# Kernel optimization log

Hardware: AMD Instinct MI355X
Metric: run time of the kernel (lower is better)

## Reference

```python
import jax, jax.numpy as jnp
import numpy as np

N, E, D_IN, D_H, D_OUT = 50000, 800000, 128, 128, 64


def _glorot(key, shape):
    fan_in, fan_out = shape[1], shape[0]
    lim = (6.0 / (fan_in + fan_out)) ** 0.5
    return jax.random.uniform(key, shape, jnp.float32, -lim, lim)


def setup_inputs() -> dict:
    key = jax.random.key(0)
    ks = jax.random.split(key, 8)
    x = jax.random.normal(ks[0], (N, D_IN), jnp.float32)
    edge_index = jax.random.randint(ks[1], (2, E), 0, N, jnp.int64)
    # SAGEConv layer 1: lin_l (on aggregated neighbors, with bias) and lin_r (root, no bias)
    W1l = _glorot(ks[2], (D_H, D_IN))
    b1 = jnp.zeros((D_H,), jnp.float32)
    W1r = _glorot(ks[3], (D_H, D_IN))
    # SAGEConv layer 2
    W2l = _glorot(ks[4], (D_OUT, D_H))
    b2 = jnp.zeros((D_OUT,), jnp.float32)
    W2r = _glorot(ks[5], (D_OUT, D_H))
    return {"x": x, "edge_index": edge_index, "W1l": W1l, "b1": b1, "W1r": W1r,
            "W2l": W2l, "b2": b2, "W2r": W2r}


def _sage_conv(x, src, dst, inv_deg, Wl, b, Wr):
    # mean-aggregate neighbor features: gather x[src], scatter-sum into dst, divide by degree
    msg_sum = jax.ops.segment_sum(x[src], dst, num_segments=N)  # [N, d]
    agg = msg_sum * inv_deg[:, None]
    return agg @ Wl.T + b + x @ Wr.T


def reference(x, edge_index, W1l, b1, W1r, W2l, b2, W2r):
    src, dst = edge_index[0], edge_index[1]
    deg = jax.ops.segment_sum(jnp.ones((E,), jnp.float32), dst, num_segments=N)
    inv_deg = jnp.where(deg > 0, 1.0 / jnp.maximum(deg, 1.0), 0.0)
    h = _sage_conv(x, src, dst, inv_deg, W1l, b1, W1r)
    h = jax.nn.relu(h)  # dropout is identity in eval mode
    out = _sage_conv(h, src, dst, inv_deg, W2l, b2, W2r)
    return out
```

## Files before the change

### kernel.cpp

```cpp
#include <hip/hip_runtime.h>
#include <hip/hip_bf16.h>

typedef __hip_bfloat16 bf16;
typedef __attribute__((ext_vector_type(8))) short short8;
typedef __attribute__((ext_vector_type(4))) float f32x4;

#define N_NODES 50000
#define NE      800000
#define DIN     128
#define DH      128
#define DOUT    64
#define MTILES  (N_NODES / 16)
#define CAP     64

__device__ __forceinline__ int clamp_node(int s) {
    return min(max(s, 0), N_NODES - 1);
}
__device__ __forceinline__ float b2f(short s) {
    unsigned u = ((unsigned)(unsigned short)s) << 16;
    float f; __builtin_memcpy(&f, &u, 4); return f;
}
__device__ __forceinline__ short f2b(float f) {
    __hip_bfloat16 h = __float2bfloat16(f);
    short s; __builtin_memcpy(&s, &h, 2); return s;
}

__global__ void k_build(const int* __restrict__ src, const int* __restrict__ dst,
                        int* __restrict__ deg, int* __restrict__ csrPad,
                        const float* __restrict__ x, __hip_bfloat162* __restrict__ xb2,
                        const float* __restrict__ W1l, const float* __restrict__ W1r,
                        const float* __restrict__ W2l, const float* __restrict__ W2r,
                        bf16* __restrict__ W1b, bf16* __restrict__ W2b) {
    int b = blockIdx.x;
    if (b < 3125) {
        int e = b * 256 + threadIdx.x;
        int t = clamp_node(dst[e]);
        int pos = atomicAdd(&deg[t], 1);
        if (pos < CAP) csrPad[t * CAP + pos] = src[e];
    } else if (b < 3125 + 6250) {
        int i = (b - 3125) * 256 + threadIdx.x;
        float4 v = ((const float4*)x)[i];
        __hip_bfloat162 a, bb;
        a.x = __float2bfloat16(v.x); a.y = __float2bfloat16(v.y);
        bb.x = __float2bfloat16(v.z); bb.y = __float2bfloat16(v.w);
        xb2[2 * i]     = a;
        xb2[2 * i + 1] = bb;
    } else {
        int i = (b - 9375) * 256 + threadIdx.x;
        if (i < 128 * 256) {
            int n = i >> 8, k = i & 255;
            float v = (k < 128) ? W1l[n * 128 + k] : W1r[n * 128 + (k - 128)];
            W1b[i] = __float2bfloat16(v);
        } else {
            int j = i - 128 * 256;
            int n = j >> 7, k = j & 127;
            float v = (n < 64) ? W2l[n * 128 + k] : W2r[(n - 64) * 128 + k];
            W2b[j] = __float2bfloat16(v);
        }
    }
}

__global__ __launch_bounds__(256) void k_agg1(const int* __restrict__ deg, const int* __restrict__ csrPad,
                                              const short* __restrict__ xb,
                                              short* __restrict__ msg) {
    int node = blockIdx.x * 4 + (threadIdx.x >> 6);
    if (node >= N_NODES) return;
    int lane = threadIdx.x & 63;
    int g = lane >> 4, c = lane & 15;
    int d = min(max(deg[node], 0), CAP);
    int lo = node * CAP, hi = lo + d;
    float acc[8];
    #pragma unroll
    for (int j = 0; j < 8; ++j) acc[j] = 0.f;
    int i = lo;
    for (; i + 7 < hi; i += 8) {
        int n0 = clamp_node(csrPad[i + g]);
        int n1 = clamp_node(csrPad[i + 4 + g]);
        short8 v0 = *(const short8*)(xb + (size_t)n0 * DIN + c * 8);
        short8 v1 = *(const short8*)(xb + (size_t)n1 * DIN + c * 8);
        #pragma unroll
        for (int j = 0; j < 8; ++j) acc[j] += b2f(v0[j]) + b2f(v1[j]);
    }
    for (; i < hi; i += 4) {
        bool valid = (i + g) < hi;
        int n = clamp_node(csrPad[valid ? (i + g) : i]);
        short8 v = *(const short8*)(xb + (size_t)n * DIN + c * 8);
        if (valid) {
            #pragma unroll
            for (int j = 0; j < 8; ++j) acc[j] += b2f(v[j]);
        }
    }
    #pragma unroll
    for (int j = 0; j < 8; ++j) {
        acc[j] += __shfl_xor(acc[j], 16);
        acc[j] += __shfl_xor(acc[j], 32);
    }
    if (g == 0) {
        float inv = (d > 0) ? 1.0f / (float)d : 0.0f;
        short8 o;
        #pragma unroll
        for (int j = 0; j < 8; ++j) o[j] = f2b(acc[j] * inv);
        *(short8*)(msg + (size_t)node * DIN + c * 8) = o;
    }
}

__global__ __launch_bounds__(256) void k_mfma12(const short* __restrict__ msg,
                                                const short* __restrict__ xb,
                                                const short* __restrict__ W1b,
                                                const float* __restrict__ b1,
                                                const short* __restrict__ W2b,
                                                bf16* __restrict__ pb,
                                                float* __restrict__ qbuf) {
    __shared__ short hs[16][136];
    int wave = threadIdx.x >> 6, lane = threadIdx.x & 63;
    int q = lane >> 4, mr = lane & 15;
    int n0 = wave * 32;
    short8 Bf1[2][8];
    #pragma unroll
    for (int t = 0; t < 2; ++t) {
        const short* wrow = W1b + (size_t)(n0 + t * 16 + mr) * 256 + q * 8;
        #pragma unroll
        for (int ks = 0; ks < 8; ++ks) Bf1[t][ks] = *(const short8*)(wrow + ks * 32);
    }
    short8 Bf2[2][4];
    #pragma unroll
    for (int t = 0; t < 2; ++t) {
        const short* wrow = W2b + (size_t)(n0 + t * 16 + mr) * 128 + q * 8;
        #pragma unroll
        for (int ks = 0; ks < 4; ++ks) Bf2[t][ks] = *(const short8*)(wrow + ks * 32);
    }
    float bias0 = b1[n0 + mr], bias1 = b1[n0 + 16 + mr];
    for (int mt = blockIdx.x; mt < MTILES; mt += gridDim.x) {
        const short* a0 = msg + (size_t)(mt * 16 + mr) * DIN + q * 8;
        const short* a1 = xb  + (size_t)(mt * 16 + mr) * DIN + q * 8;
        short8 Af[8];
        #pragma unroll
        for (int ks = 0; ks < 4; ++ks) Af[ks]     = *(const short8*)(a0 + ks * 32);
        #pragma unroll
        for (int ks = 0; ks < 4; ++ks) Af[4 + ks] = *(const short8*)(a1 + ks * 32);
        f32x4 acc0 = {0.f, 0.f, 0.f, 0.f}, acc1 = {0.f, 0.f, 0.f, 0.f};
        #pragma unroll
        for (int ks = 0; ks < 8; ++ks) {
            acc0 = __builtin_amdgcn_mfma_f32_16x16x32_bf16(Af[ks], Bf1[0][ks], acc0, 0, 0, 0);
            acc1 = __builtin_amdgcn_mfma_f32_16x16x32_bf16(Af[ks], Bf1[1][ks], acc1, 0, 0, 0);
        }
        __syncthreads();
        #pragma unroll
        for (int r = 0; r < 4; ++r) {
            int row = q * 4 + r;
            float v0 = acc0[r] + bias0;
            float v1 = acc1[r] + bias1;
            hs[row][n0 + mr]      = f2b(v0 > 0.f ? v0 : 0.f);
            hs[row][n0 + 16 + mr] = f2b(v1 > 0.f ? v1 : 0.f);
        }
        __syncthreads();
        short8 Ah[4];
        #pragma unroll
        for (int ks = 0; ks < 4; ++ks) Ah[ks] = *(const short8*)(&hs[mr][ks * 32 + q * 8]);
        f32x4 c20 = {0.f, 0.f, 0.f, 0.f}, c21 = {0.f, 0.f, 0.f, 0.f};
        #pragma unroll
        for (int ks = 0; ks < 4; ++ks) {
            c20 = __builtin_amdgcn_mfma_f32_16x16x32_bf16(Ah[ks], Bf2[0][ks], c20, 0, 0, 0);
            c21 = __builtin_amdgcn_mfma_f32_16x16x32_bf16(Ah[ks], Bf2[1][ks], c21, 0, 0, 0);
        }
        #pragma unroll
        for (int r = 0; r < 4; ++r) {
            int row = mt * 16 + q * 4 + r;
            int c0 = n0 + mr, c1 = n0 + 16 + mr;
            if (c0 < 64) {
                pb[(size_t)row * 64 + c0] = __float2bfloat16(c20[r]);
                pb[(size_t)row * 64 + c1] = __float2bfloat16(c21[r]);
            } else {
                qbuf[(size_t)row * 64 + (c0 - 64)] = c20[r];
                qbuf[(size_t)row * 64 + (c1 - 64)] = c21[r];
            }
        }
    }
}

__global__ __launch_bounds__(256) void k_agg2f(const int* __restrict__ deg, const int* __restrict__ csrPad,
                                               const short* __restrict__ pb, const float* __restrict__ qbuf,
                                               const float* __restrict__ b2, float* __restrict__ out) {
    int node = blockIdx.x * 4 + (threadIdx.x >> 6);
    if (node >= N_NODES) return;
    int lane = threadIdx.x & 63;
    int g = lane >> 3, c = lane & 7;
    int d = min(max(deg[node], 0), CAP);
    int lo = node * CAP, hi = lo + d;
    float acc[8];
    #pragma unroll
    for (int j = 0; j < 8; ++j) acc[j] = 0.f;
    int i = lo;
    for (; i + 15 < hi; i += 16) {
        int n0 = clamp_node(csrPad[i + g]);
        int n1 = clamp_node(csrPad[i + 8 + g]);
        short8 v0 = *(const short8*)(pb + (size_t)n0 * 64 + c * 8);
        short8 v1 = *(const short8*)(pb + (size_t)n1 * 64 + c * 8);
        #pragma unroll
        for (int j = 0; j < 8; ++j) acc[j] += b2f(v0[j]) + b2f(v1[j]);
    }
    for (; i < hi; i += 8) {
        bool valid = (i + g) < hi;
        int n = clamp_node(csrPad[valid ? (i + g) : i]);
        short8 v = *(const short8*)(pb + (size_t)n * 64 + c * 8);
        if (valid) {
            #pragma unroll
            for (int j = 0; j < 8; ++j) acc[j] += b2f(v[j]);
        }
    }
    #pragma unroll
    for (int j = 0; j < 8; ++j) {
        acc[j] += __shfl_xor(acc[j], 8);
        acc[j] += __shfl_xor(acc[j], 16);
        acc[j] += __shfl_xor(acc[j], 32);
    }
    if (g == 0) {
        float inv = (d > 0) ? 1.0f / (float)d : 0.0f;
        const float* qr = qbuf + (size_t)node * 64 + c * 8;
        const float* br = b2 + c * 8;
        float* orow = out + (size_t)node * 64 + c * 8;
        float4 o0, o1;
        o0.x = acc[0] * inv + qr[0] + br[0];
        o0.y = acc[1] * inv + qr[1] + br[1];
        o0.z = acc[2] * inv + qr[2] + br[2];
        o0.w = acc[3] * inv + qr[3] + br[3];
        o1.x = acc[4] * inv + qr[4] + br[4];
        o1.y = acc[5] * inv + qr[5] + br[5];
        o1.z = acc[6] * inv + qr[6] + br[6];
        o1.w = acc[7] * inv + qr[7] + br[7];
        ((float4*)orow)[0] = o0;
        ((float4*)orow)[1] = o1;
    }
}

extern "C" void kernel_launch(void* const* d_in, const int* in_sizes, int n_in,
                              void* d_out, int out_size, void* d_ws, size_t ws_size,
                              hipStream_t stream) {
    const float* x   = (const float*)d_in[0];
    const int*   ei  = (const int*)  d_in[1];
    const float* W1l = (const float*)d_in[2];
    const float* b1  = (const float*)d_in[3];
    const float* W1r = (const float*)d_in[4];
    const float* W2l = (const float*)d_in[5];
    const float* b2  = (const float*)d_in[6];
    const float* W2r = (const float*)d_in[7];
    float* out = (float*)d_out;

    const int* src = ei;
    const int* dst = ei + NE;

    char* ws = (char*)d_ws;
    int*   deg    = (int*)  (ws + 0);
    int*   csrPad = (int*)  (ws + 204800);
    short* xb     = (short*)(ws + 13004800);
    short* msg    = (short*)(ws + 25804800);
    bf16*  pb     = (bf16*) (ws + 38604800);
    float* qbuf   = (float*)(ws + 45004800);
    bf16*  W1b    = (bf16*) (ws + 57804800);
    bf16*  W2b    = (bf16*) (ws + 57870336);

    hipMemsetAsync(deg, 0, 204800, stream);

    k_build<<<9567, 256, 0, stream>>>(src, dst, deg, csrPad, x, (__hip_bfloat162*)xb,
                                      W1l, W1r, W2l, W2r, W1b, W2b);
    k_agg1<<<(N_NODES + 3) / 4, 256, 0, stream>>>(deg, csrPad, xb, msg);
    k_mfma12<<<512, 256, 0, stream>>>(msg, xb, (const short*)W1b, b1, (const short*)W2b, pb, qbuf);
    k_agg2f<<<(N_NODES + 3) / 4, 256, 0, stream>>>(deg, csrPad, (const short*)pb, qbuf, b2, out);
}
```

Before: 202.5 us.

## Store padded CSR neighbor indices as 16-bit and unroll gather loops deeper

Neighbor indices in the padded CSR are stored as unsigned 16-bit values instead of 32-bit ints, halving CSR write and read traffic. The edge-bucketing part of the build kernel now handles two edges per thread with vectorized int2 loads. Both aggregation kernels gain a four-way unrolled gather loop so more loads are in flight. Node ids reach 49999, which fits in 16 bits, so the narrower type only works because N is below 65536.

```diff
diff --git a/kernel.cpp b/kernel.cpp
--- a/kernel.cpp
+++ b/kernel.cpp
@@ -4,6 +4,7 @@
 typedef __hip_bfloat16 bf16;
 typedef __attribute__((ext_vector_type(8))) short short8;
 typedef __attribute__((ext_vector_type(4))) float f32x4;
+typedef unsigned short u16;
 
 #define N_NODES 50000
 #define NE      800000
@@ -26,19 +27,26 @@
 }
 
 __global__ void k_build(const int* __restrict__ src, const int* __restrict__ dst,
-                        int* __restrict__ deg, int* __restrict__ csrPad,
+                        int* __restrict__ deg, u16* __restrict__ csrPad,
                         const float* __restrict__ x, __hip_bfloat162* __restrict__ xb2,
                         const float* __restrict__ W1l, const float* __restrict__ W1r,
                         const float* __restrict__ W2l, const float* __restrict__ W2r,
                         bf16* __restrict__ W1b, bf16* __restrict__ W2b) {
     int b = blockIdx.x;
-    if (b < 3125) {
-        int e = b * 256 + threadIdx.x;
-        int t = clamp_node(dst[e]);
-        int pos = atomicAdd(&deg[t], 1);
-        if (pos < CAP) csrPad[t * CAP + pos] = src[e];
-    } else if (b < 3125 + 6250) {
-        int i = (b - 3125) * 256 + threadIdx.x;
+    if (b < 1563) {
+        int e0 = (b * 256 + threadIdx.x) * 2;
+        if (e0 < NE) {
+            int2 d2 = *(const int2*)(dst + e0);
+            int2 s2 = *(const int2*)(src + e0);
+            int t0 = clamp_node(d2.x);
+            int p0 = atomicAdd(&deg[t0], 1);
+            if (p0 < CAP) csrPad[t0 * CAP + p0] = (u16)s2.x;
+            int t1 = clamp_node(d2.y);
+            int p1 = atomicAdd(&deg[t1], 1);
+            if (p1 < CAP) csrPad[t1 * CAP + p1] = (u16)s2.y;
+        }
+    } else if (b < 1563 + 6250) {
+        int i = (b - 1563) * 256 + threadIdx.x;
         float4 v = ((const float4*)x)[i];
         __hip_bfloat162 a, bb;
         a.x = __float2bfloat16(v.x); a.y = __float2bfloat16(v.y);
@@ -46,7 +54,7 @@
         xb2[2 * i]     = a;
         xb2[2 * i + 1] = bb;
     } else {
-        int i = (b - 9375) * 256 + threadIdx.x;
+        int i = (b - 7813) * 256 + threadIdx.x;
         if (i < 128 * 256) {
             int n = i >> 8, k = i & 255;
             float v = (k < 128) ? W1l[n * 128 + k] : W1r[n * 128 + (k - 128)];
@@ -60,7 +68,7 @@
     }
 }
 
-__global__ __launch_bounds__(256) void k_agg1(const int* __restrict__ deg, const int* __restrict__ csrPad,
+__global__ __launch_bounds__(256) void k_agg1(const int* __restrict__ deg, const u16* __restrict__ csrPad,
                                               const short* __restrict__ xb,
                                               short* __restrict__ msg) {
     int node = blockIdx.x * 4 + (threadIdx.x >> 6);
@@ -73,6 +81,19 @@
     #pragma unroll
     for (int j = 0; j < 8; ++j) acc[j] = 0.f;
     int i = lo;
+    for (; i + 15 < hi; i += 16) {
+        int n0 = clamp_node(csrPad[i + g]);
+        int n1 = clamp_node(csrPad[i + 4 + g]);
+        int n2 = clamp_node(csrPad[i + 8 + g]);
+        int n3 = clamp_node(csrPad[i + 12 + g]);
+        short8 v0 = *(const short8*)(xb + (size_t)n0 * DIN + c * 8);
+        short8 v1 = *(const short8*)(xb + (size_t)n1 * DIN + c * 8);
+        short8 v2 = *(const short8*)(xb + (size_t)n2 * DIN + c * 8);
+        short8 v3 = *(const short8*)(xb + (size_t)n3 * DIN + c * 8);
+        #pragma unroll
+        for (int j = 0; j < 8; ++j)
+            acc[j] += (b2f(v0[j]) + b2f(v1[j])) + (b2f(v2[j]) + b2f(v3[j]));
+    }
     for (; i + 7 < hi; i += 8) {
         int n0 = clamp_node(csrPad[i + g]);
         int n1 = clamp_node(csrPad[i + 4 + g]);
@@ -178,7 +199,7 @@
     }
 }
 
-__global__ __launch_bounds__(256) void k_agg2f(const int* __restrict__ deg, const int* __restrict__ csrPad,
+__global__ __launch_bounds__(256) void k_agg2f(const int* __restrict__ deg, const u16* __restrict__ csrPad,
                                                const short* __restrict__ pb, const float* __restrict__ qbuf,
                                                const float* __restrict__ b2, float* __restrict__ out) {
     int node = blockIdx.x * 4 + (threadIdx.x >> 6);
@@ -191,6 +212,19 @@
     #pragma unroll
     for (int j = 0; j < 8; ++j) acc[j] = 0.f;
     int i = lo;
+    for (; i + 31 < hi; i += 32) {
+        int n0 = clamp_node(csrPad[i + g]);
+        int n1 = clamp_node(csrPad[i + 8 + g]);
+        int n2 = clamp_node(csrPad[i + 16 + g]);
+        int n3 = clamp_node(csrPad[i + 24 + g]);
+        short8 v0 = *(const short8*)(pb + (size_t)n0 * 64 + c * 8);
+        short8 v1 = *(const short8*)(pb + (size_t)n1 * 64 + c * 8);
+        short8 v2 = *(const short8*)(pb + (size_t)n2 * 64 + c * 8);
+        short8 v3 = *(const short8*)(pb + (size_t)n3 * 64 + c * 8);
+        #pragma unroll
+        for (int j = 0; j < 8; ++j)
+            acc[j] += (b2f(v0[j]) + b2f(v1[j])) + (b2f(v2[j]) + b2f(v3[j]));
+    }
     for (; i + 15 < hi; i += 16) {
         int n0 = clamp_node(csrPad[i + g]);
         int n1 = clamp_node(csrPad[i + 8 + g]);
@@ -251,17 +285,17 @@
 
     char* ws = (char*)d_ws;
     int*   deg    = (int*)  (ws + 0);
-    int*   csrPad = (int*)  (ws + 204800);
-    short* xb     = (short*)(ws + 13004800);
-    short* msg    = (short*)(ws + 25804800);
-    bf16*  pb     = (bf16*) (ws + 38604800);
-    float* qbuf   = (float*)(ws + 45004800);
-    bf16*  W1b    = (bf16*) (ws + 57804800);
-    bf16*  W2b    = (bf16*) (ws + 57870336);
+    u16*   csrPad = (u16*)  (ws + 204800);
+    short* xb     = (short*)(ws + 6604800);
+    short* msg    = (short*)(ws + 19404800);
+    bf16*  pb     = (bf16*) (ws + 32204800);
+    float* qbuf   = (float*)(ws + 38604800);
+    bf16*  W1b    = (bf16*) (ws + 51404800);
+    bf16*  W2b    = (bf16*) (ws + 51470336);
 
     hipMemsetAsync(deg, 0, 204800, stream);
 
-    k_build<<<9567, 256, 0, stream>>>(src, dst, deg, csrPad, x, (__hip_bfloat162*)xb,
+    k_build<<<8005, 256, 0, stream>>>(src, dst, deg, csrPad, x, (__hip_bfloat162*)xb,
                                       W1l, W1r, W2l, W2r, W1b, W2b);
     k_agg1<<<(N_NODES + 3) / 4, 256, 0, stream>>>(deg, csrPad, xb, msg);
     k_mfma12<<<512, 256, 0, stream>>>(msg, xb, (const short*)W1b, b1, (const short*)W2b, pb, qbuf);
```

Result: slower. 216.4 us (+6.8%).
